# Optimization experiments

Hardware: AMD Instinct MI355X
Metric: run time of the kernel (lower is better)

The kernel has to match this reference:

```python
import jax, jax.numpy as jnp
import numpy as np

N = 50000   # nodes
E = 800000  # edges (avg degree 16)
D = 128     # feature dim
H = 4       # heads
Dh = D // H # per-head dim = 32


def setup_inputs() -> dict:
    key = jax.random.key(0)
    ks = jax.random.split(key, 12)
    inp = {
        "x": jax.random.normal(ks[0], (N, D), jnp.float32),
        "edge_index": jax.random.randint(ks[1], (2, E), 0, N, dtype=jnp.int64),
    }
    i = 2
    for l in range(2):
        for nm in ("q", "k", "v", "s"):
            inp[f"{nm}_w{l}"] = jax.random.normal(ks[i], (D, D), jnp.float32) / np.float32(np.sqrt(D))
            inp[f"{nm}_b{l}"] = jnp.zeros((D,), jnp.float32)
        i += 1
    return inp


def _transformer_conv(x, src, dst, qw, qb, kw, kb, vw, vb, sw, sb):
    """PyG TransformerConv: concat heads, root_weight skip, softmax over in-edges."""
    n = x.shape[0]
    q = (x @ qw + qb).reshape(n, H, Dh)
    k = (x @ kw + kb).reshape(n, H, Dh)
    v = (x @ vw + vb).reshape(n, H, Dh)
    # per-edge attention logits [E, H]
    logits = jnp.einsum('ehd,ehd->eh', q[dst], k[src]) / jnp.sqrt(jnp.float32(Dh))
    # segment softmax over edges grouped by destination node
    m = jax.ops.segment_max(logits, dst, num_segments=n)          # [N, H]
    e = jnp.exp(logits - m[dst])                                  # [E, H]
    s = jax.ops.segment_sum(e, dst, num_segments=n)               # [N, H]
    alpha = e / (s[dst] + 1e-16)                                  # [E, H]
    msg = v[src] * alpha[:, :, None]                              # [E, H, Dh]
    out = jax.ops.segment_sum(msg, dst, num_segments=n)           # [N, H, Dh]
    out = out.reshape(n, H * Dh)
    return out + x @ sw + sb  # root skip (lin_skip)


def reference(x, edge_index,
              q_w0, q_b0, k_w0, k_b0, v_w0, v_b0, s_w0, s_b0,
              q_w1, q_b1, k_w1, k_b1, v_w1, v_b1, s_w1, s_b1):
    src, dst = edge_index[0], edge_index[1]
    h = _transformer_conv(x, src, dst, q_w0, q_b0, k_w0, k_b0, v_w0, v_b0, s_w0, s_b0)
    h = jax.nn.relu(h)  # dropout is identity in eval mode
    h = _transformer_conv(h, src, dst, q_w1, q_b1, k_w1, k_b1, v_w1, v_b1, s_w1, s_b1)
    return h
```

## Files before the change

### kernel.cpp

```cpp
#include <hip/hip_runtime.h>
#include <math.h>

#define NN 50000
#define NR 50016
#define EE 800000
#define SCALE 0.17677669529663687f
#define MAXDEG 64
#define NRANGE 4
#define RSPAN (NN / NRANGE)
#define NSLICE 250
#define ESLICE (EE / NSLICE)

typedef __attribute__((ext_vector_type(8))) short short8;
typedef __attribute__((ext_vector_type(4))) float floatx4;
typedef __attribute__((ext_vector_type(2))) float floatx2;
typedef __attribute__((ext_vector_type(4))) int intx4;
typedef unsigned short ushort_t;
typedef unsigned char uchar_t;

#if defined(__has_builtin)
#  if __has_builtin(__builtin_amdgcn_cvt_pk_f32_fp8)
#    define HAVE_FP8CVT 1
#  endif
#endif
#ifndef HAVE_FP8CVT
#  define HAVE_FP8CVT 0
#endif

static __device__ __forceinline__ float bf2f(ushort_t u) {
    union { unsigned int i; float f; } x; x.i = ((unsigned int)u) << 16; return x.f;
}
static __device__ __forceinline__ ushort_t f2bf(float f) {
    union { float fv; unsigned int i; } x; x.fv = f;
    unsigned int lsb = (x.i >> 16) & 1u;
    x.i += 0x7fffu + lsb;
    return (ushort_t)(x.i >> 16);
}

static __device__ __forceinline__ uchar_t f2e4m3(float f) {
    f = fminf(fmaxf(f, -448.f), 448.f);
    union { float fv; unsigned int u; } x; x.fv = f * 0x1.0p-120f;
    unsigned int lsb = (x.u >> 20) & 1u;
    x.u += 0x7FFFFu + lsb;
    return (uchar_t)(((x.u >> 24) & 0x80u) | ((x.u >> 20) & 0x7Fu));
}

static __device__ __forceinline__ float dotk16(short8 k8, const float* qf, float p) {
    union { short8 s; unsigned int u[4]; } kk; kk.s = k8;
#pragma unroll
    for (int i = 0; i < 4; ++i) {
#if HAVE_FP8CVT
        floatx2 lo = __builtin_amdgcn_cvt_pk_f32_fp8(kk.u[i], false);
        floatx2 hi = __builtin_amdgcn_cvt_pk_f32_fp8(kk.u[i], true);
        p = fmaf(lo[0], qf[4 * i + 0], p);
        p = fmaf(lo[1], qf[4 * i + 1], p);
        p = fmaf(hi[0], qf[4 * i + 2], p);
        p = fmaf(hi[1], qf[4 * i + 3], p);
#else
        unsigned int d = kk.u[i];
#pragma unroll
        for (int j = 0; j < 4; ++j) {
            unsigned int b = (d >> (8 * j)) & 0xFFu;
            union { unsigned int u; float f; } x;
            x.u = ((b & 0x80u) << 24) | ((b & 0x7Fu) << 20);
            p = fmaf(x.f * 0x1.0p+120f, qf[4 * i + j], p);
        }
#endif
    }
    return p;
}

static __device__ __forceinline__ void fma16i8(short8 v8, float ws, float* acc) {
    union { short8 s; unsigned int u[4]; } vv; vv.s = v8;
#pragma unroll
    for (int i = 0; i < 4; ++i) {
        unsigned int d = vv.u[i];
#pragma unroll
        for (int j = 0; j < 4; ++j) {
            int b = (int)(signed char)((d >> (8 * j)) & 0xFFu);
            acc[4 * i + j] = fmaf(ws, (float)b, acc[4 * i + j]);
        }
    }
}

__global__ void k_detect(const int* __restrict__ ei, int* __restrict__ flag) {
    int any = 0;
#pragma unroll
    for (int i = 0; i < 4; ++i) any |= ei[2 * (threadIdx.x * 4 + i) + 1];
    unsigned long long b = __ballot(any != 0);
    if (threadIdx.x == 0) *flag = (b == 0ull) ? 1 : 0;
}

static __device__ __forceinline__ int edge_src(const int* ei, int is64, int e) {
    return is64 ? ei[2 * e] : ei[e];
}
static __device__ __forceinline__ int edge_dst(const int* ei, int is64, int e) {
    return is64 ? ei[2 * (EE + e)] : ei[EE + e];
}

__global__ void k_prep_weights(const float* q0, const float* k0,
                               const float* v0, const float* s0,
                               const float* q1, const float* k1,
                               const float* v1, const float* s1,
                               ushort_t* wt0, ushort_t* wt1) {
    int widx = blockIdx.x >> 3;
    const float* src =
        (widx == 0) ? q0 : (widx == 1) ? k0 : (widx == 2) ? v0 : (widx == 3) ? s0 :
        (widx == 4) ? q1 : (widx == 5) ? k1 : (widx == 6) ? v1 : s1;
    ushort_t* dst = ((widx < 4) ? wt0 : wt1) + (size_t)(widx & 3) * (128 * 128);
    int it0 = (blockIdx.x & 7) * 8;
    for (int it = it0; it < it0 + 8; ++it) {
        int idx = it * 256 + threadIdx.x;
        int j    = idx & 7;
        int lane = (idx >> 3) & 63;
        int t    = (idx >> 9) & 7;
        int kkb  = idx >> 12;
        int kk = kkb * 32 + (lane >> 4) * 8 + j;
        int c  = t * 16 + (lane & 15);
        dst[idx] = f2bf(src[kk * 128 + c]);
    }
}

__global__ void k_compact(const int* __restrict__ ei, const int* __restrict__ flag,
                          int* __restrict__ pairs) {
    int e = blockIdx.x * blockDim.x + threadIdx.x;
    if (e < EE) {
        int is64 = *flag;
        pairs[2 * e]     = edge_dst(ei, is64, e);
        pairs[2 * e + 1] = edge_src(ei, is64, e);
    }
}

__global__ __launch_bounds__(256) void k_fillp(
    const int* __restrict__ pairs,
    int* __restrict__ cnt, int* __restrict__ col) {
    int range = blockIdx.x & (NRANGE - 1);
    int slice = blockIdx.x >> 2;
    int lo = range * RSPAN, hi = lo + RSPAN;
    const int* p = pairs + (size_t)slice * ESLICE * 2;
    for (int i = threadIdx.x; i < ESLICE / 2; i += 256) {
        intx4 v = *(const intx4*)(p + i * 4);
        int d0 = v[0], d1 = v[2];
        if (d0 >= lo && d0 < hi) {
            int pos = atomicAdd(&cnt[d0], 1);
            if (pos < MAXDEG) col[d0 * MAXDEG + pos] = v[1];
        }
        if (d1 >= lo && d1 < hi) {
            int pos = atomicAdd(&cnt[d1], 1);
            if (pos < MAXDEG) col[d1 * MAXDEG + pos] = v[3];
        }
    }
}

template <bool F32A>
__global__ __launch_bounds__(256) void k_gemm_qkvs(
    const void* __restrict__ Av,
    const ushort_t* __restrict__ Wp,
    const float* __restrict__ qb, const float* __restrict__ kb,
    const float* __restrict__ vb, const float* __restrict__ sb,
    ushort_t* __restrict__ Q, uchar_t* __restrict__ K8,
    uchar_t* __restrict__ V8, float* __restrict__ vscale,
    ushort_t* __restrict__ S) {
    __shared__ ushort_t sA[32][136];
    int wave = threadIdx.x >> 6;
    int lane = threadIdx.x & 63;
    int quad = lane >> 4;
    int lm = lane & 15;
    int row0 = blockIdx.x * 32;

    if (F32A) {
        int r  = threadIdx.x >> 3;
        int c0 = (threadIdx.x & 7) * 16;
        int rr = row0 + r; if (rr > NN - 1) rr = NN - 1;
        const float* srcp = (const float*)Av + (size_t)rr * 128 + c0;
        floatx4 v0 = *(const floatx4*)(srcp);
        floatx4 v1 = *(const floatx4*)(srcp + 4);
        floatx4 v2 = *(const floatx4*)(srcp + 8);
        floatx4 v3 = *(const floatx4*)(srcp + 12);
        short8 o0, o1;
#pragma unroll
        for (int i = 0; i < 4; ++i) {
            o0[i]     = (short)f2bf(v0[i]); o0[i + 4] = (short)f2bf(v1[i]);
            o1[i]     = (short)f2bf(v2[i]); o1[i + 4] = (short)f2bf(v3[i]);
        }
        *(short8*)&sA[r][c0]     = o0;
        *(short8*)&sA[r][c0 + 8] = o1;
    } else {
        const ushort_t* A = (const ushort_t*)Av;
#pragma unroll
        for (int it = 0; it < 2; ++it) {
            int r = it * 16 + (threadIdx.x >> 4);
            int c = (threadIdx.x & 15) * 8;
            *(short8*)&sA[r][c] = *(const short8*)(A + (size_t)(row0 + r) * 128 + c);
        }
    }
    __syncthreads();

    const ushort_t* wp = Wp + (size_t)wave * 16384;
    floatx4 acc[2][8];
#pragma unroll
    for (int rt = 0; rt < 2; ++rt)
#pragma unroll
        for (int t = 0; t < 8; ++t) acc[rt][t] = (floatx4)0.0f;

#pragma unroll
    for (int kkb = 0; kkb < 4; ++kkb) {
        short8 a0 = *(const short8*)&sA[lm][kkb * 32 + quad * 8];
        short8 a1 = *(const short8*)&sA[16 + lm][kkb * 32 + quad * 8];
#pragma unroll
        for (int t = 0; t < 8; ++t) {
            short8 b = *(const short8*)(wp + (size_t)((kkb * 8 + t) * 64 + lane) * 8);
            acc[0][t] = __builtin_amdgcn_mfma_f32_16x16x32_bf16(a0, b, acc[0][t], 0, 0, 0);
            acc[1][t] = __builtin_amdgcn_mfma_f32_16x16x32_bf16(a1, b, acc[1][t], 0, 0, 0);
        }
    }

    const float* bias = (wave == 0) ? qb : (wave == 1) ? kb : (wave == 2) ? vb : sb;
    if (wave == 1) {
#pragma unroll
        for (int rt = 0; rt < 2; ++rt)
#pragma unroll
            for (int t = 0; t < 8; ++t) {
                int c = t * 16 + lm;
                float bv = bias[c];
#pragma unroll
                for (int r = 0; r < 4; ++r) {
                    int row = row0 + rt * 16 + quad * 4 + r;
                    K8[(size_t)row * 128 + c] = f2e4m3(acc[rt][t][r] + bv);
                }
            }
    } else if (wave == 2) {
#pragma unroll
        for (int rt = 0; rt < 2; ++rt)
#pragma unroll
            for (int r = 0; r < 4; ++r) {
                float v[8]; float m = 0.f;
#pragma unroll
                for (int t = 0; t < 8; ++t) {
                    v[t] = acc[rt][t][r] + bias[t * 16 + lm];
                    m = fmaxf(m, fabsf(v[t]));
                }
#pragma unroll
                for (int off = 1; off <= 8; off <<= 1)
                    m = fmaxf(m, __shfl_xor(m, off));
                m = fmaxf(m, 1e-20f);
                float qs = 127.0f / m;
                int row = row0 + rt * 16 + quad * 4 + r;
                if (lm == 0) vscale[row] = m * (1.0f / 127.0f);
#pragma unroll
                for (int t = 0; t < 8; ++t) {
                    int q = (int)rintf(v[t] * qs);
                    V8[(size_t)row * 128 + t * 16 + lm] = (uchar_t)(signed char)q;
                }
            }
    } else {
        ushort_t* O = (wave == 0) ? Q : S;
#pragma unroll
        for (int rt = 0; rt < 2; ++rt)
#pragma unroll
            for (int t = 0; t < 8; ++t) {
                int c = t * 16 + lm;
                float bv = bias[c];
#pragma unroll
                for (int r = 0; r < 4; ++r) {
                    int row = row0 + rt * 16 + quad * 4 + r;
                    O[(size_t)row * 128 + c] = f2bf(acc[rt][t][r] + bv);
                }
            }
    }
}

__global__ __launch_bounds__(256) void k_attn(
    const ushort_t* __restrict__ Q, const uchar_t* __restrict__ K8,
    const uchar_t* __restrict__ V8, const float* __restrict__ vscale,
    const ushort_t* __restrict__ S,
    const int* __restrict__ cnt, const int* __restrict__ col,
    ushort_t* __restrict__ outb, float* __restrict__ outf, int do_relu) {
    int wave = threadIdx.x >> 6;
    int lane = threadIdx.x & 63;
    int nsub = lane >> 4;
    int g    = (lane >> 3) & 1;
    int sub  = lane & 7;
    int node = blockIdx.x * 16 + wave * 4 + nsub;

    const ushort_t* qrow = Q + (size_t)node * 128 + sub * 16;
    short8 qa  = *(const short8*)qrow;
    short8 qb8 = *(const short8*)(qrow + 8);

    int deg = cnt[node]; if (deg > MAXDEG) deg = MAXDEG;
    const int* crow = col + node * MAXDEG;

    int e = g;
    int s = (e < deg) ? crow[e] : 0;
    short8 k8 = *(const short8*)(K8 + (size_t)s * 128 + sub * 16);
    short8 v8 = *(const short8*)(V8 + (size_t)s * 128 + sub * 16);
    float sc = vscale[s];

    float qf[16];
#pragma unroll
    for (int i = 0; i < 8; ++i) {
        qf[i]     = bf2f((ushort_t)qa[i]);
        qf[i + 8] = bf2f((ushort_t)qb8[i]);
    }

    float l = 0.f;
    float acc[16];
#pragma unroll
    for (int i = 0; i < 16; ++i) acc[i] = 0.f;

    while (e < deg) {
        int e2 = e + 2;
        int s2 = (e2 < deg) ? crow[e2] : 0;
        short8 k8n = *(const short8*)(K8 + (size_t)s2 * 128 + sub * 16);
        short8 v8n = *(const short8*)(V8 + (size_t)s2 * 128 + sub * 16);
        float scn = vscale[s2];

        float p = dotk16(k8, qf, 0.f);
        p += __shfl_xor(p, 1);
        float w = __expf(p * SCALE);
        l += w;
        fma16i8(v8, w * sc, acc);

        e = e2; s = s2; k8 = k8n; v8 = v8n; sc = scn;
    }

    l += __shfl_xor(l, 8);
#pragma unroll
    for (int i = 0; i < 16; ++i) acc[i] += __shfl_xor(acc[i], 8);

    if (g == 0) {
        float inv = 1.0f / (l + 1e-16f);
        const ushort_t* srow = S + (size_t)node * 128 + sub * 16;
        short8 sa = *(const short8*)srow;
        short8 sb8 = *(const short8*)(srow + 8);
        float o[16];
#pragma unroll
        for (int i = 0; i < 8; ++i) {
            o[i]     = acc[i]     * inv + bf2f((ushort_t)sa[i]);
            o[i + 8] = acc[i + 8] * inv + bf2f((ushort_t)sb8[i]);
        }
        if (do_relu)
#pragma unroll
            for (int i = 0; i < 16; ++i) o[i] = fmaxf(o[i], 0.f);
        if (outb) {
            short8 ob0, ob1;
#pragma unroll
            for (int i = 0; i < 8; ++i) {
                ob0[i] = (short)f2bf(o[i]);
                ob1[i] = (short)f2bf(o[i + 8]);
            }
            *(short8*)(outb + (size_t)node * 128 + sub * 16)     = ob0;
            *(short8*)(outb + (size_t)node * 128 + sub * 16 + 8) = ob1;
        }
        if (outf) {
#pragma unroll
            for (int t = 0; t < 4; ++t) {
                floatx4 ov;
#pragma unroll
                for (int i = 0; i < 4; ++i) ov[i] = o[t * 4 + i];
                *(floatx4*)(outf + (size_t)node * 128 + sub * 16 + t * 4) = ov;
            }
        }
    }
}

extern "C" void kernel_launch(void* const* d_in, const int* in_sizes, int n_in,
                              void* d_out, int out_size, void* d_ws, size_t ws_size,
                              hipStream_t stream) {
    const float* x  = (const float*)d_in[0];
    const int*   ei = (const int*)d_in[1];
    const float* qw0 = (const float*)d_in[2];
    const float* qb0 = (const float*)d_in[3];
    const float* kw0 = (const float*)d_in[4];
    const float* kb0 = (const float*)d_in[5];
    const float* vw0 = (const float*)d_in[6];
    const float* vb0 = (const float*)d_in[7];
    const float* sw0 = (const float*)d_in[8];
    const float* sb0 = (const float*)d_in[9];
    const float* qw1 = (const float*)d_in[10];
    const float* qb1 = (const float*)d_in[11];
    const float* kw1 = (const float*)d_in[12];
    const float* kb1 = (const float*)d_in[13];
    const float* vw1 = (const float*)d_in[14];
    const float* vb1 = (const float*)d_in[15];
    const float* sw1 = (const float*)d_in[16];
    const float* sb1 = (const float*)d_in[17];

    char* ws = (char*)d_ws;
    size_t off = 0;
    auto alloc = [&](size_t bytes) -> void* {
        void* p = ws + off;
        off = (off + bytes + 255) & ~(size_t)255;
        return p;
    };
    int* flag       = (int*)alloc(4);
    int* cnt        = (int*)alloc((size_t)NN * 4);
    int* pairs      = (int*)alloc((size_t)EE * 8);
    int* colp       = (int*)alloc((size_t)NN * MAXDEG * 4);
    ushort_t* wt0   = (ushort_t*)alloc((size_t)512 * 128 * 2);
    ushort_t* wt1   = (ushort_t*)alloc((size_t)512 * 128 * 2);
    ushort_t* Q     = (ushort_t*)alloc((size_t)NR * 128 * 2);
    uchar_t*  K8    = (uchar_t*)alloc((size_t)NR * 128);
    uchar_t*  V8    = (uchar_t*)alloc((size_t)NR * 128);
    float*    vscale= (float*)alloc((size_t)NR * 4);
    ushort_t* S     = (ushort_t*)alloc((size_t)NR * 128 * 2);
    ushort_t* h1b   = (ushort_t*)alloc((size_t)NR * 128 * 2);
    (void)ws_size; (void)in_sizes; (void)n_in; (void)out_size;

    (void)hipMemsetAsync(cnt, 0, (size_t)NN * 4, stream);
    k_detect<<<1, 64, 0, stream>>>(ei, flag);
    k_prep_weights<<<64, 256, 0, stream>>>(qw0, kw0, vw0, sw0, qw1, kw1, vw1, sw1, wt0, wt1);
    k_compact<<<(EE + 255) / 256, 256, 0, stream>>>(ei, flag, pairs);
    k_fillp<<<NSLICE * NRANGE, 256, 0, stream>>>(pairs, cnt, colp);

    k_gemm_qkvs<true><<<NR / 32, 256, 0, stream>>>(x, wt0, qb0, kb0, vb0, sb0,
                                                   Q, K8, V8, vscale, S);
    k_attn<<<NN / 16, 256, 0, stream>>>(Q, K8, V8, vscale, S, cnt, colp,
                                        h1b, nullptr, 1);

    k_gemm_qkvs<false><<<NR / 32, 256, 0, stream>>>(h1b, wt1, qb1, kb1, vb1, sb1,
                                                    Q, K8, V8, vscale, S);
    k_attn<<<NN / 16, 256, 0, stream>>>(Q, K8, V8, vscale, S, cnt, colp,
                                        nullptr, (float*)d_out, 0);
}
```

Before: 276.4 us.

## Simplify CSR fill, use packed conversions, and bias V to unsigned int8

The CSR fill kernel drops its four-range partitioning, which made every block scan its edge slice four times. It now uses one pass over edges, with each edge atomically bumping the counter of its own destination. GEMM epilogues and the attention output use the hardware packed bf16 and fp8 conversion instructions in place of manual bit rounding. V is stored as unsigned (q+128), so the attention inner loop skips sign extension, and a single correction term (128 times the weight sum) is subtracted at the end. The trade-offs are more contention on the atomic counters with less locality, and a small numeric change from the offset correction.

```diff
diff --git a/kernel.cpp b/kernel.cpp
--- a/kernel.cpp
+++ b/kernel.cpp
@@ -6,10 +6,8 @@
 #define EE 800000
 #define SCALE 0.17677669529663687f
 #define MAXDEG 64
-#define NRANGE 4
-#define RSPAN (NN / NRANGE)
-#define NSLICE 250
-#define ESLICE (EE / NSLICE)
+#define FBLK 1000
+#define EPB (EE / FBLK)
 
 typedef __attribute__((ext_vector_type(8))) short short8;
 typedef __attribute__((ext_vector_type(4))) float floatx4;
@@ -22,9 +20,15 @@
 #  if __has_builtin(__builtin_amdgcn_cvt_pk_f32_fp8)
 #    define HAVE_FP8CVT 1
 #  endif
+#  if __has_builtin(__builtin_amdgcn_cvt_pk_fp8_f32)
+#    define HAVE_FP8PK 1
+#  endif
 #endif
 #ifndef HAVE_FP8CVT
 #  define HAVE_FP8CVT 0
+#endif
+#ifndef HAVE_FP8PK
+#  define HAVE_FP8PK 0
 #endif
 
 static __device__ __forceinline__ float bf2f(ushort_t u) {
@@ -35,6 +39,12 @@
     unsigned int lsb = (x.i >> 16) & 1u;
     x.i += 0x7fffu + lsb;
     return (ushort_t)(x.i >> 16);
+}
+
+static __device__ __forceinline__ unsigned int pk_bf16(float a, float b) {
+    unsigned int r;
+    asm("v_cvt_pk_bf16_f32 %0, %1, %2" : "=v"(r) : "v"(a), "v"(b));
+    return r;
 }
 
 static __device__ __forceinline__ uchar_t f2e4m3(float f) {
@@ -70,15 +80,15 @@
     return p;
 }
 
-static __device__ __forceinline__ void fma16i8(short8 v8, float ws, float* acc) {
+static __device__ __forceinline__ void fma16u8(short8 v8, float ws, float* acc) {
     union { short8 s; unsigned int u[4]; } vv; vv.s = v8;
 #pragma unroll
     for (int i = 0; i < 4; ++i) {
         unsigned int d = vv.u[i];
 #pragma unroll
         for (int j = 0; j < 4; ++j) {
-            int b = (int)(signed char)((d >> (8 * j)) & 0xFFu);
-            acc[4 * i + j] = fmaf(ws, (float)b, acc[4 * i + j]);
+            float u = (float)((d >> (8 * j)) & 0xFFu);
+            acc[4 * i + j] = fmaf(ws, u, acc[4 * i + j]);
         }
     }
 }
@@ -134,21 +144,13 @@
 __global__ __launch_bounds__(256) void k_fillp(
     const int* __restrict__ pairs,
     int* __restrict__ cnt, int* __restrict__ col) {
-    int range = blockIdx.x & (NRANGE - 1);
-    int slice = blockIdx.x >> 2;
-    int lo = range * RSPAN, hi = lo + RSPAN;
-    const int* p = pairs + (size_t)slice * ESLICE * 2;
-    for (int i = threadIdx.x; i < ESLICE / 2; i += 256) {
+    const int* p = pairs + (size_t)blockIdx.x * EPB * 2;
+    for (int i = threadIdx.x; i < EPB / 2; i += 256) {
         intx4 v = *(const intx4*)(p + i * 4);
-        int d0 = v[0], d1 = v[2];
-        if (d0 >= lo && d0 < hi) {
-            int pos = atomicAdd(&cnt[d0], 1);
-            if (pos < MAXDEG) col[d0 * MAXDEG + pos] = v[1];
-        }
-        if (d1 >= lo && d1 < hi) {
-            int pos = atomicAdd(&cnt[d1], 1);
-            if (pos < MAXDEG) col[d1 * MAXDEG + pos] = v[3];
-        }
+        int pos0 = atomicAdd(&cnt[v[0]], 1);
+        if (pos0 < MAXDEG) col[v[0] * MAXDEG + pos0] = v[1];
+        int pos1 = atomicAdd(&cnt[v[2]], 1);
+        if (pos1 < MAXDEG) col[v[2] * MAXDEG + pos1] = v[3];
     }
 }
 
@@ -177,14 +179,13 @@
         floatx4 v1 = *(const floatx4*)(srcp + 4);
         floatx4 v2 = *(const floatx4*)(srcp + 8);
         floatx4 v3 = *(const floatx4*)(srcp + 12);
-        short8 o0, o1;
-#pragma unroll
-        for (int i = 0; i < 4; ++i) {
-            o0[i]     = (short)f2bf(v0[i]); o0[i + 4] = (short)f2bf(v1[i]);
-            o1[i]     = (short)f2bf(v2[i]); o1[i + 4] = (short)f2bf(v3[i]);
-        }
-        *(short8*)&sA[r][c0]     = o0;
-        *(short8*)&sA[r][c0 + 8] = o1;
+        union { short8 s; unsigned int u[4]; } o0, o1;
+        o0.u[0] = pk_bf16(v0[0], v0[1]); o0.u[1] = pk_bf16(v0[2], v0[3]);
+        o0.u[2] = pk_bf16(v1[0], v1[1]); o0.u[3] = pk_bf16(v1[2], v1[3]);
+        o1.u[0] = pk_bf16(v2[0], v2[1]); o1.u[1] = pk_bf16(v2[2], v2[3]);
+        o1.u[2] = pk_bf16(v3[0], v3[1]); o1.u[3] = pk_bf16(v3[2], v3[3]);
+        *(short8*)&sA[r][c0]     = o0.s;
+        *(short8*)&sA[r][c0 + 8] = o1.s;
     } else {
         const ushort_t* A = (const ushort_t*)Av;
 #pragma unroll
@@ -220,13 +221,24 @@
 #pragma unroll
         for (int rt = 0; rt < 2; ++rt)
 #pragma unroll
-            for (int t = 0; t < 8; ++t) {
-                int c = t * 16 + lm;
-                float bv = bias[c];
+            for (int t = 0; t < 8; t += 2) {
+                float b0v = bias[t * 16 + lm];
+                float b1v = bias[(t + 1) * 16 + lm];
 #pragma unroll
                 for (int r = 0; r < 4; ++r) {
                     int row = row0 + rt * 16 + quad * 4 + r;
-                    K8[(size_t)row * 128 + c] = f2e4m3(acc[rt][t][r] + bv);
+                    uchar_t* bp = K8 + (size_t)row * 128 + t * 16 + lm;
+                    float a = acc[rt][t][r] + b0v;
+                    float b = acc[rt][t + 1][r] + b1v;
+#if HAVE_FP8PK
+                    unsigned int pk =
+                        (unsigned int)__builtin_amdgcn_cvt_pk_fp8_f32(a, b, 0, false);
+                    bp[0]  = (uchar_t)pk;
+                    bp[16] = (uchar_t)(pk >> 8);
+#else
+                    bp[0]  = f2e4m3(a);
+                    bp[16] = f2e4m3(b);
+#endif
                 }
             }
     } else if (wave == 2) {
@@ -250,7 +262,7 @@
 #pragma unroll
                 for (int t = 0; t < 8; ++t) {
                     int q = (int)rintf(v[t] * qs);
-                    V8[(size_t)row * 128 + t * 16 + lm] = (uchar_t)(signed char)q;
+                    V8[(size_t)row * 128 + t * 16 + lm] = (uchar_t)(q + 128);
                 }
             }
     } else {
@@ -258,13 +270,17 @@
 #pragma unroll
         for (int rt = 0; rt < 2; ++rt)
 #pragma unroll
-            for (int t = 0; t < 8; ++t) {
-                int c = t * 16 + lm;
-                float bv = bias[c];
+            for (int t = 0; t < 8; t += 2) {
+                float b0v = bias[t * 16 + lm];
+                float b1v = bias[(t + 1) * 16 + lm];
 #pragma unroll
                 for (int r = 0; r < 4; ++r) {
                     int row = row0 + rt * 16 + quad * 4 + r;
-                    O[(size_t)row * 128 + c] = f2bf(acc[rt][t][r] + bv);
+                    unsigned int pk = pk_bf16(acc[rt][t][r] + b0v,
+                                              acc[rt][t + 1][r] + b1v);
+                    ushort_t* bp = O + (size_t)row * 128 + t * 16 + lm;
+                    bp[0]  = (ushort_t)pk;
+                    bp[16] = (ushort_t)(pk >> 16);
                 }
             }
     }
@@ -303,7 +319,7 @@
         qf[i + 8] = bf2f((ushort_t)qb8[i]);
     }
 
-    float l = 0.f;
+    float l = 0.f, wssum = 0.f;
     float acc[16];
 #pragma unroll
     for (int i = 0; i < 16; ++i) acc[i] = 0.f;
@@ -319,38 +335,42 @@
         p += __shfl_xor(p, 1);
         float w = __expf(p * SCALE);
         l += w;
-        fma16i8(v8, w * sc, acc);
+        float ws = w * sc;
+        wssum += ws;
+        fma16u8(v8, ws, acc);
 
         e = e2; s = s2; k8 = k8n; v8 = v8n; sc = scn;
     }
 
     l += __shfl_xor(l, 8);
+    wssum += __shfl_xor(wssum, 8);
 #pragma unroll
     for (int i = 0; i < 16; ++i) acc[i] += __shfl_xor(acc[i], 8);
 
     if (g == 0) {
         float inv = 1.0f / (l + 1e-16f);
+        float corr = 128.0f * wssum;
         const ushort_t* srow = S + (size_t)node * 128 + sub * 16;
         short8 sa = *(const short8*)srow;
         short8 sb8 = *(const short8*)(srow + 8);
         float o[16];
 #pragma unroll
         for (int i = 0; i < 8; ++i) {
-            o[i]     = acc[i]     * inv + bf2f((ushort_t)sa[i]);
-            o[i + 8] = acc[i + 8] * inv + bf2f((ushort_t)sb8[i]);
+            o[i]     = (acc[i]     - corr) * inv + bf2f((ushort_t)sa[i]);
+            o[i + 8] = (acc[i + 8] - corr) * inv + bf2f((ushort_t)sb8[i]);
         }
         if (do_relu)
 #pragma unroll
             for (int i = 0; i < 16; ++i) o[i] = fmaxf(o[i], 0.f);
         if (outb) {
-            short8 ob0, ob1;
-#pragma unroll
-            for (int i = 0; i < 8; ++i) {
-                ob0[i] = (short)f2bf(o[i]);
-                ob1[i] = (short)f2bf(o[i + 8]);
+            union { short8 s; unsigned int u[4]; } ob0, ob1;
+#pragma unroll
+            for (int i = 0; i < 4; ++i) {
+                ob0.u[i] = pk_bf16(o[2 * i],     o[2 * i + 1]);
+                ob1.u[i] = pk_bf16(o[8 + 2 * i], o[8 + 2 * i + 1]);
             }
-            *(short8*)(outb + (size_t)node * 128 + sub * 16)     = ob0;
-            *(short8*)(outb + (size_t)node * 128 + sub * 16 + 8) = ob1;
+            *(short8*)(outb + (size_t)node * 128 + sub * 16)     = ob0.s;
+            *(short8*)(outb + (size_t)node * 128 + sub * 16 + 8) = ob1.s;
         }
         if (outf) {
 #pragma unroll
@@ -411,7 +431,7 @@
     k_detect<<<1, 64, 0, stream>>>(ei, flag);
     k_prep_weights<<<64, 256, 0, stream>>>(qw0, kw0, vw0, sw0, qw1, kw1, vw1, sw1, wt0, wt1);
     k_compact<<<(EE + 255) / 256, 256, 0, stream>>>(ei, flag, pairs);
-    k_fillp<<<NSLICE * NRANGE, 256, 0, stream>>>(pairs, cnt, colp);
+    k_fillp<<<FBLK, 256, 0, stream>>>(pairs, cnt, colp);
 
     k_gemm_qkvs<true><<<NR / 32, 256, 0, stream>>>(x, wt0, qb0, kb0, vb0, sb0,
                                                    Q, K8, V8, vscale, S);
```

Measured after the change: 283.7 us. 1.03x slower.
